# Kernel tuning notes

Measured on AMD Instinct MI355X. Metric: run time of the kernel, lower is better.

## Reference

```python
import jax, jax.numpy as jnp
import numpy as np

D = 1024      # model_dim
H = 2048      # expert hidden_dim
E = 8         # num routed experts
TOP_K = 2
N_SHARED = 1
B, S = 2, 1024


def setup_inputs() -> dict:
    key = jax.random.key(0)
    ks = jax.random.split(key, 12)
    sc = 0.02
    return {
        "hidden": jax.random.normal(ks[0], (B, S, D), jnp.float32),
        # router Linear(D -> E); stored as [in, out]
        "router_w": jax.random.normal(ks[1], (D, E), jnp.float32) * sc,
        "router_b": jnp.zeros((E,), jnp.float32),
        # shared expert (1): Linear(D->H), Linear(H->D)
        "sw1": jax.random.normal(ks[2], (D, H), jnp.float32) * sc,
        "sb1": jnp.zeros((H,), jnp.float32),
        "sw2": jax.random.normal(ks[3], (H, D), jnp.float32) * sc,
        "sb2": jnp.zeros((D,), jnp.float32),
        # routed experts, stacked over E
        "rw1": jax.random.normal(ks[4], (E, D, H), jnp.float32) * sc,
        "rb1": jnp.zeros((E, H), jnp.float32),
        "rw2": jax.random.normal(ks[5], (E, H, D), jnp.float32) * sc,
        "rb2": jnp.zeros((E, D), jnp.float32),
    }


def reference(hidden, router_w, router_b, sw1, sb1, sw2, sb2, rw1, rb1, rw2, rb2):
    b, s, d = hidden.shape
    T = b * s
    flat = hidden.reshape(T, d)                              # [T, D]

    # --- router ---
    router_logits = flat @ router_w + router_b               # [T, E]
    router_probs = jax.nn.softmax(router_logits, axis=-1)
    topk_probs, topk_idx = jax.lax.top_k(router_probs, TOP_K)  # [T, K]

    # per-(token, expert) mixing weight: sum of top-k probs that hit expert e
    weights = jnp.zeros_like(router_probs).at[
        jnp.arange(T)[:, None], topk_idx
    ].add(topk_probs)                                        # [T, E]

    # --- shared expert(s) (1 expert -> mean == itself) ---
    sh = jax.nn.gelu(flat @ sw1 + sb1, approximate=False)    # [T, H]
    shared_out = (sh @ sw2 + sb2) / N_SHARED                 # [T, D]

    # --- routed experts: dense all-expert eval weighted by routing weights ---
    # (identical math to the gather/FFN/index_add loop: weight is 0 for
    #  tokens not routed to expert e)
    h1 = jax.nn.gelu(jnp.einsum('td,edh->teh', flat, rw1) + rb1[None],
                     approximate=False)                      # [T, E, H]
    expert_out = jnp.einsum('teh,ehd->ted', h1, rw2) + rb2[None]  # [T, E, D]
    mixed = jnp.einsum('ted,te->td', expert_out, weights)    # [T, D]

    return (shared_out + mixed).reshape(b, s, d)
```

## Files before the change

### kernel.cpp

```cpp
#include <hip/hip_runtime.h>
#include <hip/hip_bf16.h>

#define T_TOK 2048
#define DDIM  1024
#define HDIM  2048
#define NEXP  8
#define NSEG  9

typedef unsigned short u16;
typedef __attribute__((ext_vector_type(4))) float f32x4;
typedef __attribute__((ext_vector_type(8))) short bf16x8;
typedef __attribute__((ext_vector_type(4))) unsigned short u16x4;
typedef __attribute__((ext_vector_type(8))) unsigned short u16x8;

__device__ __forceinline__ u16 f2bf(float x) {
  union { float f; unsigned int u; } v; v.f = x;
  unsigned int r = v.u + 0x7fffu + ((v.u >> 16) & 1u);
  return (u16)(r >> 16);
}
__device__ __forceinline__ float gelu_fast(float x) {
  float y = x * (1.595769122f + 0.0713548162f * x * x);
  return x / (1.0f + __expf(-y));
}
__device__ __forceinline__ int swz4(int row) {
  return (row & 3) ^ ((row >> 2) & 3);
}

__device__ __forceinline__ void gload16(const void* g, void* l) {
  __builtin_amdgcn_global_load_lds(
      (const __attribute__((address_space(1))) unsigned int*)g,
      (__attribute__((address_space(3))) unsigned int*)l, 16, 0, 0);
}

__global__ __launch_bounds__(256) void router_kernel(
    const float* __restrict__ x, const float* __restrict__ rw,
    const float* __restrict__ rb, u16* __restrict__ xb,
    float* __restrict__ weights, int* __restrict__ counts,
    int* __restrict__ lists)
{
  int wv = threadIdx.x >> 6, lane = threadIdx.x & 63;
  int t = blockIdx.x * 4 + wv;
  const float* xrow = x + (size_t)t * DDIM;
  float acc[NEXP];
#pragma unroll
  for (int e = 0; e < NEXP; e++) acc[e] = 0.f;
#pragma unroll
  for (int i = 0; i < 4; i++) {
    int d0 = i * 256 + lane * 4;
    f32x4 xv = *(const f32x4*)(xrow + d0);
    u16x4 pk;
#pragma unroll
    for (int j = 0; j < 4; j++) {
      float xs = xv[j];
      pk[j] = f2bf(xs);
      const float* wr = rw + (size_t)(d0 + j) * NEXP;
#pragma unroll
      for (int e = 0; e < NEXP; e++) acc[e] = fmaf(xs, wr[e], acc[e]);
    }
    *(u16x4*)(xb + (size_t)t * DDIM + d0) = pk;
  }
#pragma unroll
  for (int off = 32; off >= 1; off >>= 1)
#pragma unroll
    for (int e = 0; e < NEXP; e++) acc[e] += __shfl_xor(acc[e], off);

  if (lane == 0) {
    float lg[NEXP], mx = -1e30f;
#pragma unroll
    for (int e = 0; e < NEXP; e++) { lg[e] = acc[e] + rb[e]; mx = fmaxf(mx, lg[e]); }
    float p[NEXP], s = 0.f;
#pragma unroll
    for (int e = 0; e < NEXP; e++) { p[e] = expf(lg[e] - mx); s += p[e]; }
    float inv = 1.0f / s;
#pragma unroll
    for (int e = 0; e < NEXP; e++) p[e] *= inv;
    int i1 = 0;
#pragma unroll
    for (int e = 1; e < NEXP; e++) if (p[e] > p[i1]) i1 = e;
    int i2 = (i1 == 0) ? 1 : 0;
#pragma unroll
    for (int e = 0; e < NEXP; e++) if (e != i1 && p[e] > p[i2]) i2 = e;
#pragma unroll
    for (int e = 0; e < NEXP; e++)
      weights[(size_t)t * NEXP + e] = (e == i1) ? p[i1] : (e == i2) ? p[i2] : 0.f;
    int p1 = atomicAdd(counts + i1, 1); lists[i1 * T_TOK + p1] = t;
    int p2 = atomicAdd(counts + i2, 1); lists[i2 * T_TOK + p2] = t;
    lists[NEXP * T_TOK + t] = t;
  }
}

__global__ void seg_kernel(int* counts, int* segoff, int* ytab, int* nyt) {
  counts[NEXP] = T_TOK;
  int off = 0, n = 0;
  for (int e = 0; e < NSEG; e++) {
    segoff[e] = off;
    int c = counts[e];
    for (int my = 0; my * 256 < c; my++) ytab[n++] = e * 256 + my;
    off += c;
  }
  *nyt = n;
}

__global__ __launch_bounds__(512) void gemm1_kernel(
    const u16* __restrict__ Xb, const float* __restrict__ rw1,
    const float* __restrict__ sw1, const float* __restrict__ rb1,
    const float* __restrict__ sb1, const int* __restrict__ counts,
    const int* __restrict__ segoff, const int* __restrict__ lists,
    const int* __restrict__ ytab, const int* __restrict__ nyt,
    u16* __restrict__ H1)
{
  __shared__ u16 Alds[256 * 64];
  __shared__ u16 Blds[128 * 64];

  int tid = threadIdx.x, lane = tid & 63;
  int wv = tid >> 6, wm = wv >> 1, wn = wv & 1;
  int kc = lane >> 4, lr = lane & 15;

  int srow[4], achk[4];
#pragma unroll
  for (int r = 0; r < 4; r++) {
    int i = r * 512 + tid;
    srow[r] = i >> 3;
    achk[r] = ((i & 7) ^ ((i >> 3) & 7)) * 8;
  }
  int aoff[2][4], boff[2][4];
#pragma unroll
  for (int ks = 0; ks < 2; ks++)
#pragma unroll
    for (int f = 0; f < 4; f++) {
      int ra = wm * 64 + f * 16 + lr;
      int rb_ = wn * 64 + f * 16 + lr;
      aoff[ks][f] = ra * 64 + (((ks * 4 + kc) ^ (ra & 7)) * 8);
      boff[ks][f] = rb_ * 64 + (((ks * 4 + kc) ^ (rb_ & 7)) * 8);
    }
  int bchk = (wv ^ (lane & 7)) * 8;

  int ntile = nyt[0] * (HDIM / 128);
  for (int t = blockIdx.x; t < ntile; t += gridDim.x) {
    int yt = t >> 4, nx = t & 15;
    int em = ytab[yt];
    int e = em >> 8, m0 = (em & 255) * 256, n0 = nx * 128;
    int cnt = counts[e];
    const float* Wf = (e < NEXP) ? (rw1 + (size_t)e * DDIM * HDIM) : sw1;
    const float* bias = (e < NEXP) ? (rb1 + (size_t)e * HDIM) : sb1;
    const int* list = lists + e * T_TOK;
    int seg = segoff[e];

    size_t asrc[4];
#pragma unroll
    for (int r = 0; r < 4; r++) {
      int tok = list[min(m0 + srow[r], cnt - 1)];
      asrc[r] = (size_t)tok * DDIM + achk[r];
    }
    const float* Wbase = Wf + n0 + lane;

    f32x4 acc[4][4];
#pragma unroll
    for (int i = 0; i < 4; i++)
#pragma unroll
      for (int j = 0; j < 4; j++) acc[i][j] = (f32x4){0.f, 0.f, 0.f, 0.f};

    float vb0[8], vb1[8];
    {
      const float* Wk = Wbase + (size_t)(wv * 8) * HDIM;
#pragma unroll
      for (int q = 0; q < 8; q++) {
        vb0[q] = Wk[(size_t)q * HDIM];
        vb1[q] = Wk[(size_t)q * HDIM + 64];
      }
    }

    const int NS = DDIM / 64;
    for (int s = 0; s < NS; s++) {
      int kk = s * 64;
#pragma unroll
      for (int r = 0; r < 4; r++)
        gload16(Xb + asrc[r] + kk, Alds + (size_t)(r * 512 + tid) * 8);
      {
        u16x8 pk0, pk1;
#pragma unroll
        for (int q = 0; q < 8; q++) { pk0[q] = f2bf(vb0[q]); pk1[q] = f2bf(vb1[q]); }
        *(u16x8*)(Blds + (size_t)lane * 64 + bchk) = pk0;
        *(u16x8*)(Blds + (size_t)(lane + 64) * 64 + bchk) = pk1;
      }
      __syncthreads();
      if (s + 1 < NS) {
        const float* Wk = Wbase + (size_t)((s + 1) * 64 + wv * 8) * HDIM;
#pragma unroll
        for (int q = 0; q < 8; q++) {
          vb0[q] = Wk[(size_t)q * HDIM];
          vb1[q] = Wk[(size_t)q * HDIM + 64];
        }
      }
#pragma unroll
      for (int ks = 0; ks < 2; ks++) {
        bf16x8 af[4], bfr[4];
#pragma unroll
        for (int f = 0; f < 4; f++) {
          af[f]  = *(const bf16x8*)(Alds + aoff[ks][f]);
          bfr[f] = *(const bf16x8*)(Blds + boff[ks][f]);
        }
#pragma unroll
        for (int mf = 0; mf < 4; mf++)
#pragma unroll
          for (int nf = 0; nf < 4; nf++)
            acc[mf][nf] = __builtin_amdgcn_mfma_f32_16x16x32_bf16(af[mf], bfr[nf], acc[mf][nf], 0, 0, 0);
      }
      __syncthreads();
    }

#pragma unroll
    for (int nf = 0; nf < 4; nf++) {
      int col = n0 + wn * 64 + nf * 16 + lr;
      float b = bias[col];
#pragma unroll
      for (int mf = 0; mf < 4; mf++) {
#pragma unroll
        for (int rg = 0; rg < 4; rg++) {
          int mt = wm * 64 + mf * 16 + kc * 4 + rg;
          if (m0 + mt < cnt) {
            float v = acc[mf][nf][rg] + b;
            H1[(size_t)(seg + m0 + mt) * HDIM + col] = f2bf(gelu_fast(v));
          }
        }
      }
    }
  }
}

__global__ __launch_bounds__(512) void gemm2_kernel(
    const u16* __restrict__ H1, const float* __restrict__ rw2,
    const float* __restrict__ sw2, const float* __restrict__ rb2,
    const float* __restrict__ sb2, const float* __restrict__ weights,
    const int* __restrict__ counts, const int* __restrict__ segoff,
    const int* __restrict__ lists, const int* __restrict__ ytab,
    const int* __restrict__ nyt, float* __restrict__ out)
{
  __shared__ u16 Alds[4][256 * 32];
  __shared__ u16 Blds[2][256 * 32];

  int tid = threadIdx.x, lane = tid & 63;
  int wv = tid >> 6, wm = wv >> 2, wn = wv & 3;
  int kc = lane >> 4, lr = lane & 15;

  int srow[2], soff[2];
#pragma unroll
  for (int j = 0; j < 2; j++) {
    int i = j * 512 + tid;
    srow[j] = i >> 2;
    soff[j] = (((i & 3) ^ swz4(i >> 2)) * 8);
  }
  int aoff[8], boff[4];
#pragma unroll
  for (int f = 0; f < 8; f++) {
    int ra = wm * 128 + f * 16 + lr;
    aoff[f] = ra * 32 + ((kc ^ swz4(ra)) * 8);
  }
#pragma unroll
  for (int f = 0; f < 4; f++) {
    int rb_ = wn * 64 + f * 16 + lr;
    boff[f] = rb_ * 32 + ((kc ^ swz4(rb_)) * 8);
  }
  int brow = lane + (wv & 3) * 64;
  int bh   = wv >> 2;
  int bws  = swz4(brow);
  int bc0 = ((bh * 2) ^ bws) * 8;
  int bc1 = ((bh * 2 + 1) ^ bws) * 8;

  int ntile = nyt[0] * (DDIM / 256) * 2;
  for (int t = blockIdx.x; t < ntile; t += gridDim.x) {
    int kh = t & 1, nx = (t >> 1) & 3, yt = t >> 3;
    int em = ytab[yt];
    int e = em >> 8, m0 = (em & 255) * 256, n0 = nx * 256;
    int cnt = counts[e];
    const float* Wf = (e < NEXP) ? (rw2 + (size_t)e * HDIM * DDIM) : sw2;
    const float* bias = (e < NEXP) ? (rb2 + (size_t)e * DDIM) : sb2;
    const int* list = lists + e * T_TOK;
    int seg = segoff[e];
    int k0 = kh * 1024;

    size_t abase[2];
#pragma unroll
    for (int j = 0; j < 2; j++)
      abase[j] = (size_t)(seg + min(m0 + srow[j], cnt - 1)) * HDIM + k0 + soff[j];
    const float* Wb2 = Wf + (size_t)k0 * DDIM + n0 + brow;

    f32x4 acc[8][4];
#pragma unroll
    for (int i = 0; i < 8; i++)
#pragma unroll
      for (int j = 0; j < 4; j++) acc[i][j] = (f32x4){0.f, 0.f, 0.f, 0.f};

    const int NS = 1024 / 32;
    float vb[16];
    {
      const float* Wk = Wb2 + (size_t)(bh * 16) * DDIM;
#pragma unroll
      for (int q = 0; q < 16; q++) vb[q] = Wk[(size_t)q * DDIM];
    }
#pragma unroll
    for (int s = 0; s < 2; s++)
#pragma unroll
      for (int j = 0; j < 2; j++) {
        int i = j * 512 + tid;
        gload16(H1 + abase[j] + s * 32, &Alds[s][i * 8]);
      }

    for (int s = 0; s < NS; s++) {
      if (s + 2 < NS) {
        int kk = (s + 2) * 32;
        int nb = (s + 2) & 3;
#pragma unroll
        for (int j = 0; j < 2; j++) {
          int i = j * 512 + tid;
          gload16(H1 + abase[j] + kk, &Alds[nb][i * 8]);
        }
      }
      {
        u16* Bd = &Blds[s & 1][0];
        u16x8 pk0, pk1;
#pragma unroll
        for (int q = 0; q < 8; q++) { pk0[q] = f2bf(vb[q]); pk1[q] = f2bf(vb[q + 8]); }
        *(u16x8*)(Bd + (size_t)brow * 32 + bc0) = pk0;
        *(u16x8*)(Bd + (size_t)brow * 32 + bc1) = pk1;
      }
      if (s + 1 < NS) {
        const float* Wk = Wb2 + (size_t)((s + 1) * 32 + bh * 16) * DDIM;
#pragma unroll
        for (int q = 0; q < 16; q++) vb[q] = Wk[(size_t)q * DDIM];
      }
      if (s + 2 < NS)      asm volatile("s_waitcnt vmcnt(18)" ::: "memory");
      else if (s + 1 < NS) asm volatile("s_waitcnt vmcnt(16)" ::: "memory");
      else                 asm volatile("s_waitcnt vmcnt(0)" ::: "memory");
      asm volatile("s_waitcnt lgkmcnt(0)" ::: "memory");
      __builtin_amdgcn_s_barrier();
      __builtin_amdgcn_sched_barrier(0);

      const u16* Ac = &Alds[s & 3][0];
      const u16* Bc = &Blds[s & 1][0];
      bf16x8 af[8], bfr[4];
#pragma unroll
      for (int f = 0; f < 8; f++) af[f] = *(const bf16x8*)(Ac + aoff[f]);
#pragma unroll
      for (int f = 0; f < 4; f++) bfr[f] = *(const bf16x8*)(Bc + boff[f]);
      __builtin_amdgcn_s_setprio(1);
#pragma unroll
      for (int mf = 0; mf < 8; mf++)
#pragma unroll
        for (int nf = 0; nf < 4; nf++)
          acc[mf][nf] = __builtin_amdgcn_mfma_f32_16x16x32_bf16(af[mf], bfr[nf], acc[mf][nf], 0, 0, 0);
      __builtin_amdgcn_s_setprio(0);
    }

    float biasv[4];
#pragma unroll
    for (int nf = 0; nf < 4; nf++)
      biasv[nf] = (kh == 0) ? bias[n0 + wn * 64 + nf * 16 + lr] : 0.f;

#pragma unroll
    for (int mf = 0; mf < 8; mf++) {
#pragma unroll
      for (int rg = 0; rg < 4; rg++) {
        int mt = wm * 128 + mf * 16 + kc * 4 + rg;
        int mrow = m0 + mt;
        if (mrow < cnt) {
          int tok = list[mrow];
          float w = (e < NEXP) ? weights[(size_t)tok * NEXP + e] : 1.0f;
          float* orow = out + (size_t)tok * DDIM + n0 + wn * 64 + lr;
#pragma unroll
          for (int nf = 0; nf < 4; nf++)
            atomicAdd(orow + nf * 16, w * (acc[mf][nf][rg] + biasv[nf]));
        }
      }
    }
    __builtin_amdgcn_s_barrier();
    __builtin_amdgcn_sched_barrier(0);
  }
}

extern "C" void kernel_launch(void* const* d_in, const int* in_sizes, int n_in,
                              void* d_out, int out_size, void* d_ws, size_t ws_size,
                              hipStream_t stream) {
  (void)in_sizes; (void)n_in; (void)out_size; (void)ws_size;
  const float* hidden   = (const float*)d_in[0];
  const float* router_w = (const float*)d_in[1];
  const float* router_b = (const float*)d_in[2];
  const float* sw1 = (const float*)d_in[3];
  const float* sb1 = (const float*)d_in[4];
  const float* sw2 = (const float*)d_in[5];
  const float* sb2 = (const float*)d_in[6];
  const float* rw1 = (const float*)d_in[7];
  const float* rb1 = (const float*)d_in[8];
  const float* rw2 = (const float*)d_in[9];
  const float* rb2 = (const float*)d_in[10];
  float* out = (float*)d_out;

  char* ws = (char*)d_ws;
  u16* Xb      = (u16*)(ws + 0);
  u16* H1      = (u16*)(ws + 4194304);
  float* weights = (float*)(ws + 29360128);
  int* counts  = (int*)(ws + 29425664);
  int* segoff  = (int*)(ws + 29425728);
  int* lists   = (int*)(ws + 29425792);
  int* ytab    = (int*)(ws + 29499520);
  int* nyt     = (int*)(ws + 29500160);

  hipMemsetAsync(counts, 0, 64, stream);
  hipMemsetAsync(out, 0, (size_t)T_TOK * DDIM * sizeof(float), stream);

  router_kernel<<<T_TOK / 4, 256, 0, stream>>>(hidden, router_w, router_b, Xb,
                                               weights, counts, lists);
  seg_kernel<<<1, 1, 0, stream>>>(counts, segoff, ytab, nyt);

  gemm1_kernel<<<512, 512, 0, stream>>>(
      Xb, rw1, sw1, rb1, sb1, counts, segoff, lists, ytab, nyt, H1);
  gemm2_kernel<<<256, 512, 0, stream>>>(
      H1, rw2, sw2, rb2, sb2, weights, counts, segoff, lists, ytab, nyt, out);
}
```

Measured before the change: 225.7 us.

## Narrow gemm2 output tile to 256x128 and raise grid to 384 blocks

Cuts the gemm2 N tile from 256 to 128 columns, so the 8 waves now form a 4x2 layout, each owning a 64x64 sub-tile. Each thread loads and converts 8 fp32 weights per k-step instead of 16, and the wait counts are adjusted to match. The grid grows from 256 to 384 blocks to spread the doubled number of tiles. This is meant to cut per-thread register pressure and B-load latency and to improve load balance across CUs, at the cost of reloading the A tile twice as often per output.

New measurement: 226.3 us. About the same (+0.3%).

```diff
diff --git a/kernel.cpp b/kernel.cpp
--- a/kernel.cpp
+++ b/kernel.cpp
@@ -237,10 +237,10 @@
     const int* __restrict__ nyt, float* __restrict__ out)
 {
   __shared__ u16 Alds[4][256 * 32];
-  __shared__ u16 Blds[2][256 * 32];
+  __shared__ u16 Blds[2][128 * 32];
 
   int tid = threadIdx.x, lane = tid & 63;
-  int wv = tid >> 6, wm = wv >> 2, wn = wv & 3;
+  int wv = tid >> 6, wm = wv >> 1, wn = wv & 1;
   int kc = lane >> 4, lr = lane & 15;
 
   int srow[2], soff[2];
@@ -250,28 +250,22 @@
     srow[j] = i >> 2;
     soff[j] = (((i & 3) ^ swz4(i >> 2)) * 8);
   }
-  int aoff[8], boff[4];
-#pragma unroll
-  for (int f = 0; f < 8; f++) {
-    int ra = wm * 128 + f * 16 + lr;
+  int aoff[4], boff[4];
+#pragma unroll
+  for (int f = 0; f < 4; f++) {
+    int ra = wm * 64 + f * 16 + lr;
+    int rb_ = wn * 64 + f * 16 + lr;
     aoff[f] = ra * 32 + ((kc ^ swz4(ra)) * 8);
-  }
-#pragma unroll
-  for (int f = 0; f < 4; f++) {
-    int rb_ = wn * 64 + f * 16 + lr;
     boff[f] = rb_ * 32 + ((kc ^ swz4(rb_)) * 8);
   }
-  int brow = lane + (wv & 3) * 64;
-  int bh   = wv >> 2;
-  int bws  = swz4(brow);
-  int bc0 = ((bh * 2) ^ bws) * 8;
-  int bc1 = ((bh * 2 + 1) ^ bws) * 8;
-
-  int ntile = nyt[0] * (DDIM / 256) * 2;
+  int brow = tid & 127, bc = tid >> 7;
+  int bwo = (size_t)0 + brow * 32 + ((bc ^ swz4(brow)) * 8);
+
+  int ntile = nyt[0] * (DDIM / 128) * 2;
   for (int t = blockIdx.x; t < ntile; t += gridDim.x) {
-    int kh = t & 1, nx = (t >> 1) & 3, yt = t >> 3;
+    int kh = t & 1, nx = (t >> 1) & 7, yt = t >> 4;
     int em = ytab[yt];
-    int e = em >> 8, m0 = (em & 255) * 256, n0 = nx * 256;
+    int e = em >> 8, m0 = (em & 255) * 256, n0 = nx * 128;
     int cnt = counts[e];
     const float* Wf = (e < NEXP) ? (rw2 + (size_t)e * HDIM * DDIM) : sw2;
     const float* bias = (e < NEXP) ? (rb2 + (size_t)e * DDIM) : sb2;
@@ -283,21 +277,18 @@
 #pragma unroll
     for (int j = 0; j < 2; j++)
       abase[j] = (size_t)(seg + min(m0 + srow[j], cnt - 1)) * HDIM + k0 + soff[j];
-    const float* Wb2 = Wf + (size_t)k0 * DDIM + n0 + brow;
-
-    f32x4 acc[8][4];
-#pragma unroll
-    for (int i = 0; i < 8; i++)
+    const float* Wb2 = Wf + (size_t)(k0 + bc * 8) * DDIM + n0 + brow;
+
+    f32x4 acc[4][4];
+#pragma unroll
+    for (int i = 0; i < 4; i++)
 #pragma unroll
       for (int j = 0; j < 4; j++) acc[i][j] = (f32x4){0.f, 0.f, 0.f, 0.f};
 
     const int NS = 1024 / 32;
-    float vb[16];
-    {
-      const float* Wk = Wb2 + (size_t)(bh * 16) * DDIM;
-#pragma unroll
-      for (int q = 0; q < 16; q++) vb[q] = Wk[(size_t)q * DDIM];
-    }
+    float vb[8];
+#pragma unroll
+    for (int q = 0; q < 8; q++) vb[q] = Wb2[(size_t)q * DDIM];
 #pragma unroll
     for (int s = 0; s < 2; s++)
 #pragma unroll
@@ -317,20 +308,18 @@
         }
       }
       {
-        u16* Bd = &Blds[s & 1][0];
-        u16x8 pk0, pk1;
-#pragma unroll
-        for (int q = 0; q < 8; q++) { pk0[q] = f2bf(vb[q]); pk1[q] = f2bf(vb[q + 8]); }
-        *(u16x8*)(Bd + (size_t)brow * 32 + bc0) = pk0;
-        *(u16x8*)(Bd + (size_t)brow * 32 + bc1) = pk1;
+        u16x8 pk;
+#pragma unroll
+        for (int q = 0; q < 8; q++) pk[q] = f2bf(vb[q]);
+        *(u16x8*)(&Blds[s & 1][0] + bwo) = pk;
       }
       if (s + 1 < NS) {
-        const float* Wk = Wb2 + (size_t)((s + 1) * 32 + bh * 16) * DDIM;
-#pragma unroll
-        for (int q = 0; q < 16; q++) vb[q] = Wk[(size_t)q * DDIM];
-      }
-      if (s + 2 < NS)      asm volatile("s_waitcnt vmcnt(18)" ::: "memory");
-      else if (s + 1 < NS) asm volatile("s_waitcnt vmcnt(16)" ::: "memory");
+        const float* Wk = Wb2 + (size_t)((s + 1) * 32) * DDIM;
+#pragma unroll
+        for (int q = 0; q < 8; q++) vb[q] = Wk[(size_t)q * DDIM];
+      }
+      if (s + 2 < NS)      asm volatile("s_waitcnt vmcnt(10)" ::: "memory");
+      else if (s + 1 < NS) asm volatile("s_waitcnt vmcnt(8)" ::: "memory");
       else                 asm volatile("s_waitcnt vmcnt(0)" ::: "memory");
       asm volatile("s_waitcnt lgkmcnt(0)" ::: "memory");
       __builtin_amdgcn_s_barrier();
@@ -338,14 +327,15 @@
 
       const u16* Ac = &Alds[s & 3][0];
       const u16* Bc = &Blds[s & 1][0];
-      bf16x8 af[8], bfr[4];
-#pragma unroll
-      for (int f = 0; f < 8; f++) af[f] = *(const bf16x8*)(Ac + aoff[f]);
-#pragma unroll
-      for (int f = 0; f < 4; f++) bfr[f] = *(const bf16x8*)(Bc + boff[f]);
+      bf16x8 af[4], bfr[4];
+#pragma unroll
+      for (int f = 0; f < 4; f++) {
+        af[f]  = *(const bf16x8*)(Ac + aoff[f]);
+        bfr[f] = *(const bf16x8*)(Bc + boff[f]);
+      }
       __builtin_amdgcn_s_setprio(1);
 #pragma unroll
-      for (int mf = 0; mf < 8; mf++)
+      for (int mf = 0; mf < 4; mf++)
 #pragma unroll
         for (int nf = 0; nf < 4; nf++)
           acc[mf][nf] = __builtin_amdgcn_mfma_f32_16x16x32_bf16(af[mf], bfr[nf], acc[mf][nf], 0, 0, 0);
@@ -358,10 +348,10 @@
       biasv[nf] = (kh == 0) ? bias[n0 + wn * 64 + nf * 16 + lr] : 0.f;
 
 #pragma unroll
-    for (int mf = 0; mf < 8; mf++) {
+    for (int mf = 0; mf < 4; mf++) {
 #pragma unroll
       for (int rg = 0; rg < 4; rg++) {
-        int mt = wm * 128 + mf * 16 + kc * 4 + rg;
+        int mt = wm * 64 + mf * 16 + kc * 4 + rg;
         int mrow = m0 + mt;
         if (mrow < cnt) {
           int tok = list[mrow];
@@ -414,6 +404,6 @@
 
   gemm1_kernel<<<512, 512, 0, stream>>>(
       Xb, rw1, sw1, rb1, sb1, counts, segoff, lists, ytab, nyt, H1);
-  gemm2_kernel<<<256, 512, 0, stream>>>(
+  gemm2_kernel<<<384, 512, 0, stream>>>(
       H1, rw2, sw2, rb2, sb2, weights, counts, segoff, lists, ytab, nyt, out);
 }
```
